# Performance work log

Measured on AMD Instinct MI355X. Metric: run time of the kernel, lower is better.

Reference implementation:

```python
import jax, jax.numpy as jnp
import numpy as np

N_ATOMS = 1048576
N_CRYS = 8192
NFEA = 128
NCLS = 5
LN_EPS = 1e-5


def setup_inputs() -> dict:
    key = jax.random.key(0)
    k1, k2, k3 = jax.random.split(key, 3)
    data_crys_fea = jax.random.normal(k1, (N_ATOMS, NFEA), dtype=jnp.float32)
    # Contiguous non-empty [start, end) ranges partitioning [0, N_ATOMS)
    rng = np.random.default_rng(0)
    cuts = np.sort(rng.choice(np.arange(1, N_ATOMS), size=N_CRYS - 1, replace=False))
    starts = np.concatenate([[0], cuts])
    ends = np.concatenate([cuts, [N_ATOMS]])
    data_crys_idx = jnp.asarray(np.stack([starts, ends], axis=1).astype(np.int32))
    ln_weight = jnp.ones((NFEA,), dtype=jnp.float32)
    ln_bias = jnp.zeros((NFEA,), dtype=jnp.float32)
    out_w = jax.random.normal(k2, (NCLS, NFEA), dtype=jnp.float32) / np.sqrt(NFEA).astype(np.float32)
    out_b = jax.random.normal(k3, (NCLS,), dtype=jnp.float32) * 0.01
    return {
        "data_crys_fea": data_crys_fea,
        "data_crys_idx": data_crys_idx,
        "ln_weight": ln_weight,
        "ln_bias": ln_bias,
        "out_w": out_w,
        "out_b": out_b,
    }


def reference(data_crys_fea, data_crys_idx, ln_weight, ln_bias, out_w, out_b):
    # --- pool: per-crystal mean over contiguous [start, end) atom ranges ---
    starts = data_crys_idx[:, 0]
    ends = data_crys_idx[:, 1]
    n_atoms = data_crys_fea.shape[0]
    # segment id of each atom via searchsorted on sorted starts
    seg = jnp.searchsorted(starts, jnp.arange(n_atoms, dtype=starts.dtype), side="right") - 1
    seg_sum = jax.ops.segment_sum(data_crys_fea, seg, num_segments=N_CRYS)  # [n_crys, F]
    lens = (ends - starts).astype(data_crys_fea.dtype)
    pooled = seg_sum / lens[:, None]
    # --- LayerNorm over features (biased variance, eps=1e-5, like torch) ---
    mu = jnp.mean(pooled, axis=-1, keepdims=True)
    var = jnp.var(pooled, axis=-1, keepdims=True)
    normed = (pooled - mu) / jnp.sqrt(var + LN_EPS) * ln_weight + ln_bias
    # --- Softplus then Linear ---
    act = jax.nn.softplus(normed)  # [n_crys, F]
    my_output = act @ out_w.T + out_b  # [n_crys, n_cls]
    return my_output, act
```

## Files before the change

kernel.cpp:

```cpp
#include <hip/hip_runtime.h>
#include <hip/hip_bf16.h>

#define NFEA 128
#define NCLS 5
#define LN_EPS 1e-5f
#define CHUNK 256

typedef float f32x4 __attribute__((ext_vector_type(4)));

__device__ __forceinline__ void finalize_vec(
    int lane, int fc, int c, f32x4 sum, float inv_len,
    const float* __restrict__ lnw, const float* __restrict__ lnb,
    const float* __restrict__ outw, const float* __restrict__ outb,
    float* __restrict__ out_cls, float* __restrict__ out_act)
{
    f32x4 p;
    p[0] = sum[0] * inv_len; p[1] = sum[1] * inv_len;
    p[2] = sum[2] * inv_len; p[3] = sum[3] * inv_len;

    float t = p[0] + p[1] + p[2] + p[3];
    #pragma unroll
    for (int off = 16; off; off >>= 1) t += __shfl_xor(t, off);
    const float mu = t * (1.f / NFEA);

    f32x4 d;
    d[0] = p[0] - mu; d[1] = p[1] - mu; d[2] = p[2] - mu; d[3] = p[3] - mu;
    float v = d[0]*d[0] + d[1]*d[1] + d[2]*d[2] + d[3]*d[3];
    #pragma unroll
    for (int off = 16; off; off >>= 1) v += __shfl_xor(v, off);
    const float rstd = rsqrtf(v * (1.f / NFEA) + LN_EPS);

    const f32x4 w4 = ((const f32x4*)lnw)[fc];
    const f32x4 b4 = ((const f32x4*)lnb)[fc];
    f32x4 act;
    #pragma unroll
    for (int j = 0; j < 4; ++j) {
        const float x = d[j] * rstd * w4[j] + b4[j];
        act[j] = (x > 0.f) ? x + log1pf(expf(-x)) : log1pf(expf(x));
    }
    if (lane < 32) ((f32x4*)out_act)[(size_t)c * 32 + fc] = act;

    #pragma unroll
    for (int k = 0; k < NCLS; ++k) {
        const f32x4 wk = ((const f32x4*)outw)[k * 32 + fc];
        float pk = act[0]*wk[0] + act[1]*wk[1] + act[2]*wk[2] + act[3]*wk[3];
        #pragma unroll
        for (int off = 16; off; off >>= 1) pk += __shfl_xor(pk, off);
        if (lane == k) out_cls[(size_t)c * NCLS + k] = pk + outb[k];
    }
}

__global__ __launch_bounds__(256) void prep_kernel(
    const int2* __restrict__ idx,
    int*  __restrict__ seg_of_chunk,
    float* __restrict__ seg_sum,
    int n_crys)
{
    const int t    = blockIdx.x * 256 + threadIdx.x;
    const int nthr = gridDim.x * 256;

    f32x4* z = (f32x4*)seg_sum;
    const int nz = n_crys * NFEA / 4;
    for (int i = t; i < nz; i += nthr) z[i] = (f32x4){0.f, 0.f, 0.f, 0.f};

    if (t < n_crys) {
        const int2 se = idx[t];
        int j = (se.x + CHUNK - 1) / CHUNK;
        for (; j * CHUNK < se.y; ++j) seg_of_chunk[j] = t;
    }
}

__global__ __launch_bounds__(256) void seg_sum_kernel(
    const float* __restrict__ fea,
    const int2*  __restrict__ idx,
    const int*   __restrict__ seg_of_chunk,
    float* __restrict__ seg_sum)
{
    const int c0 = blockIdx.x * CHUNK;
    const int c1 = c0 + CHUNK;
    const int tid = threadIdx.x;
    const int fc  = tid & 31;
    const int al  = tid >> 5;

    int s = seg_of_chunk[blockIdx.x];
    const f32x4* __restrict__ fea4 = (const f32x4*)fea;
    __shared__ f32x4 red4[8][32];

    int rs = c0;
    while (rs < c1) {
        const int re = min(idx[s].y, c1);

        f32x4 acc0 = {0.f,0.f,0.f,0.f};
        f32x4 acc1 = {0.f,0.f,0.f,0.f};
        f32x4 acc2 = {0.f,0.f,0.f,0.f};
        f32x4 acc3 = {0.f,0.f,0.f,0.f};

        int a = rs + al;
        if (a + 24 < re) {
            f32x4 v0 = fea4[(size_t)a        * 32 + fc];
            f32x4 v1 = fea4[(size_t)(a + 8)  * 32 + fc];
            f32x4 v2 = fea4[(size_t)(a + 16) * 32 + fc];
            f32x4 v3 = fea4[(size_t)(a + 24) * 32 + fc];
            a += 32;
            for (; a + 24 < re; a += 32) {
                f32x4 n0 = fea4[(size_t)a        * 32 + fc];
                f32x4 n1 = fea4[(size_t)(a + 8)  * 32 + fc];
                f32x4 n2 = fea4[(size_t)(a + 16) * 32 + fc];
                f32x4 n3 = fea4[(size_t)(a + 24) * 32 + fc];
                acc0 += v0; acc1 += v1; acc2 += v2; acc3 += v3;
                v0 = n0; v1 = n1; v2 = n2; v3 = n3;
            }
            acc0 += v0; acc1 += v1; acc2 += v2; acc3 += v3;
        }
        for (; a < re; a += 8)
            acc0 += fea4[(size_t)a * 32 + fc];

        f32x4 accT = (acc0 + acc1) + (acc2 + acc3);

        red4[al][fc] = accT;
        __syncthreads();
        if (tid < NFEA) {
            const float* redf = (const float*)red4;
            float ssum = 0.f;
            #pragma unroll
            for (int g = 0; g < 8; ++g) ssum += redf[g * NFEA + tid];
            atomicAdd(&seg_sum[(size_t)s * NFEA + tid], ssum);
        }
        __syncthreads();
        rs = re; ++s;
    }
}

__global__ __launch_bounds__(256) void finalize_kernel(
    const float* __restrict__ seg_sum,
    const int2*  __restrict__ idx,
    const float* __restrict__ lnw, const float* __restrict__ lnb,
    const float* __restrict__ outw, const float* __restrict__ outb,
    float* __restrict__ out_cls, float* __restrict__ out_act,
    int n_crys)
{
    const int c    = (blockIdx.x * 256 + threadIdx.x) >> 6;
    const int lane = threadIdx.x & 63;
    if (c >= n_crys) return;
    const int2 se = idx[c];
    const int fc = lane & 31;
    const f32x4 sum = ((const f32x4*)seg_sum)[(size_t)c * 32 + fc];
    finalize_vec(lane, fc, c, sum, 1.f / (float)(se.y - se.x),
                 lnw, lnb, outw, outb, out_cls, out_act);
}

extern "C" void kernel_launch(void* const* d_in, const int* in_sizes, int n_in,
                              void* d_out, int out_size, void* d_ws, size_t ws_size,
                              hipStream_t stream) {
    const float* fea  = (const float*)d_in[0];
    const int2*  idx  = (const int2*)d_in[1];
    const float* lnw  = (const float*)d_in[2];
    const float* lnb  = (const float*)d_in[3];
    const float* outw = (const float*)d_in[4];
    const float* outb = (const float*)d_in[5];

    const int n_crys  = in_sizes[1] / 2;
    const int n_atoms = in_sizes[0] / NFEA;
    const int nchunk  = n_atoms / CHUNK;

    float* seg_sum      = (float*)d_ws;
    int*   seg_of_chunk = (int*)((char*)d_ws + (size_t)n_crys * NFEA * sizeof(float));

    float* out_cls = (float*)d_out;
    float* out_act = (float*)d_out + (size_t)n_crys * NCLS;

    prep_kernel<<<256, 256, 0, stream>>>(idx, seg_of_chunk, seg_sum, n_crys);
    seg_sum_kernel<<<nchunk, 256, 0, stream>>>(fea, idx, seg_of_chunk, seg_sum);
    finalize_kernel<<<(n_crys + 3) / 4, 256, 0, stream>>>(
        seg_sum, idx, lnw, lnb, outw, outb, out_cls, out_act, n_crys);
}
```

Before: 133.3 us.

## Make segment-sum kernel persistent with double-buffered shared reduction

Replaces the one-block-per-chunk launch with a fixed grid of 2048 blocks that grid-stride over the 256-atom chunks. The shared reduction buffer is double-buffered so the second barrier per segment can be dropped. The load unroll is cut from four to two accumulators, lowering register pressure. The tradeoff is less memory-level parallelism per wave and the correctness burden of the ping-pong buffer scheme.

```diff
diff --git a/kernel.cpp b/kernel.cpp
--- a/kernel.cpp
+++ b/kernel.cpp
@@ -5,6 +5,7 @@
 #define NCLS 5
 #define LN_EPS 1e-5f
 #define CHUNK 256
+#define NBLK 2048
 
 typedef float f32x4 __attribute__((ext_vector_type(4)));
 
@@ -74,60 +75,57 @@
     const float* __restrict__ fea,
     const int2*  __restrict__ idx,
     const int*   __restrict__ seg_of_chunk,
-    float* __restrict__ seg_sum)
+    float* __restrict__ seg_sum,
+    int nchunk)
 {
-    const int c0 = blockIdx.x * CHUNK;
-    const int c1 = c0 + CHUNK;
     const int tid = threadIdx.x;
     const int fc  = tid & 31;
     const int al  = tid >> 5;
 
-    int s = seg_of_chunk[blockIdx.x];
     const f32x4* __restrict__ fea4 = (const f32x4*)fea;
-    __shared__ f32x4 red4[8][32];
+    __shared__ f32x4 red4[2][8][32];
+    int p = 0;
 
-    int rs = c0;
-    while (rs < c1) {
-        const int re = min(idx[s].y, c1);
+    for (int j = blockIdx.x; j < nchunk; j += gridDim.x) {
+        const int c0 = j * CHUNK;
+        const int c1 = c0 + CHUNK;
+        int s  = seg_of_chunk[j];
+        int rs = c0;
 
-        f32x4 acc0 = {0.f,0.f,0.f,0.f};
-        f32x4 acc1 = {0.f,0.f,0.f,0.f};
-        f32x4 acc2 = {0.f,0.f,0.f,0.f};
-        f32x4 acc3 = {0.f,0.f,0.f,0.f};
+        while (rs < c1) {
+            const int re = min(idx[s].y, c1);
 
-        int a = rs + al;
-        if (a + 24 < re) {
-            f32x4 v0 = fea4[(size_t)a        * 32 + fc];
-            f32x4 v1 = fea4[(size_t)(a + 8)  * 32 + fc];
-            f32x4 v2 = fea4[(size_t)(a + 16) * 32 + fc];
-            f32x4 v3 = fea4[(size_t)(a + 24) * 32 + fc];
-            a += 32;
-            for (; a + 24 < re; a += 32) {
-                f32x4 n0 = fea4[(size_t)a        * 32 + fc];
-                f32x4 n1 = fea4[(size_t)(a + 8)  * 32 + fc];
-                f32x4 n2 = fea4[(size_t)(a + 16) * 32 + fc];
-                f32x4 n3 = fea4[(size_t)(a + 24) * 32 + fc];
-                acc0 += v0; acc1 += v1; acc2 += v2; acc3 += v3;
-                v0 = n0; v1 = n1; v2 = n2; v3 = n3;
+            f32x4 acc0 = {0.f,0.f,0.f,0.f};
+            f32x4 acc1 = {0.f,0.f,0.f,0.f};
+
+            int a = rs + al;
+            if (a + 8 < re) {
+                f32x4 v0 = fea4[(size_t)a       * 32 + fc];
+                f32x4 v1 = fea4[(size_t)(a + 8) * 32 + fc];
+                a += 16;
+                for (; a + 8 < re; a += 16) {
+                    f32x4 n0 = fea4[(size_t)a       * 32 + fc];
+                    f32x4 n1 = fea4[(size_t)(a + 8) * 32 + fc];
+                    acc0 += v0; acc1 += v1;
+                    v0 = n0; v1 = n1;
+                }
+                acc0 += v0; acc1 += v1;
             }
-            acc0 += v0; acc1 += v1; acc2 += v2; acc3 += v3;
+            for (; a < re; a += 8)
+                acc0 += fea4[(size_t)a * 32 + fc];
+
+            red4[p][al][fc] = acc0 + acc1;
+            __syncthreads();
+            if (tid < NFEA) {
+                const float* redf = (const float*)red4[p];
+                float ssum = 0.f;
+                #pragma unroll
+                for (int g = 0; g < 8; ++g) ssum += redf[g * NFEA + tid];
+                atomicAdd(&seg_sum[(size_t)s * NFEA + tid], ssum);
+            }
+            p ^= 1;
+            rs = re; ++s;
         }
-        for (; a < re; a += 8)
-            acc0 += fea4[(size_t)a * 32 + fc];
-
-        f32x4 accT = (acc0 + acc1) + (acc2 + acc3);
-
-        red4[al][fc] = accT;
-        __syncthreads();
-        if (tid < NFEA) {
-            const float* redf = (const float*)red4;
-            float ssum = 0.f;
-            #pragma unroll
-            for (int g = 0; g < 8; ++g) ssum += redf[g * NFEA + tid];
-            atomicAdd(&seg_sum[(size_t)s * NFEA + tid], ssum);
-        }
-        __syncthreads();
-        rs = re; ++s;
     }
 }
 
@@ -170,7 +168,7 @@
     float* out_act = (float*)d_out + (size_t)n_crys * NCLS;
 
     prep_kernel<<<256, 256, 0, stream>>>(idx, seg_of_chunk, seg_sum, n_crys);
-    seg_sum_kernel<<<nchunk, 256, 0, stream>>>(fea, idx, seg_of_chunk, seg_sum);
+    seg_sum_kernel<<<NBLK, 256, 0, stream>>>(fea, idx, seg_of_chunk, seg_sum, nchunk);
     finalize_kernel<<<(n_crys + 3) / 4, 256, 0, stream>>>(
         seg_sum, idx, lnw, lnb, outw, outb, out_cls, out_act, n_crys);
 }
```

After: 133.5 us. Within noise of the previous version (+0.2%).
